# Optimization experiments

Measured on AMD Instinct MI355X. Metric: run time of the kernel, lower is better.

The kernel has to match this reference:

```python
import jax, jax.numpy as jnp
import numpy as np

N_NODES = 50000
N_EDGES = 500000
L_DIM = 128
MAX_ETYPES = 5
SELF_ETYPE = 4  # hardcoded in compute_edge_attention
K_FRAC = 0.5


def setup_inputs() -> dict:
    key = jax.random.key(0)
    ks = jax.random.split(key, 12)
    h = jax.random.normal(ks[0], (N_NODES, L_DIM), jnp.float32)
    src = jax.random.randint(ks[1], (N_EDGES,), 0, N_NODES)
    off = jax.random.randint(ks[2], (N_EDGES,), 1, N_NODES)
    dst = (src + off) % N_NODES  # guaranteed self-loop-free (remove_self_loop is a no-op)
    etype = jax.random.randint(ks[3], (N_EDGES,), 0, MAX_ETYPES)
    s = 0.05
    W_bases = jax.random.normal(ks[4], (2, 2 * L_DIM, L_DIM), jnp.float32) * s  # basis weights
    coeff = jax.random.normal(ks[5], (MAX_ETYPES, 2), jnp.float32)              # per-type basis coeffs
    Wq = jax.random.normal(ks[6], (L_DIM, L_DIM), jnp.float32) * s
    bq = jnp.zeros((L_DIM,), jnp.float32)
    Wk = jax.random.normal(ks[7], (L_DIM, L_DIM), jnp.float32) * s
    bk = jnp.zeros((L_DIM,), jnp.float32)
    Wv = jax.random.normal(ks[8], (1, L_DIM), jnp.float32) * s
    bv = jnp.zeros((1,), jnp.float32)
    return {"h": h, "src": src, "dst": dst, "etype": etype,
            "W_bases": W_bases, "coeff": coeff,
            "Wq": Wq, "bq": bq, "Wk": Wk, "bk": bk, "Wv": Wv, "bv": bv}


def typed_linear(x, et, W_bases, coeff):
    # basis-decomposed typed linear: W(t) = coeff[t,0]*W0 + coeff[t,1]*W1
    xW0 = x @ W_bases[0]
    xW1 = x @ W_bases[1]
    c = coeff[et]  # [E, 2]
    return c[:, 0:1] * xW0 + c[:, 1:2] * xW1


def reference(h, src, dst, etype, W_bases, coeff, Wq, bq, Wk, bk, Wv, bv):
    n, d = h.shape
    scale = jnp.sqrt(jnp.asarray(d, h.dtype))
    # self contribution: typed_linear([h, h], etype=4) -> w_v
    self_et = jnp.full((n,), SELF_ETYPE, dtype=jnp.int32)
    self_y = typed_linear(jnp.concatenate([h, h], axis=1), self_et, W_bases, coeff) @ Wv.T + bv  # [N,1]
    n_q = h @ Wq.T + bq  # [N, d]

    def direction(s_idx, d_idx):
        z2 = jnp.concatenate([h[s_idx], h[d_idx]], axis=1)          # [E, 2d]
        emb = typed_linear(z2, etype, W_bases, coeff)               # [E, d]
        n_k = emb @ Wk.T + bk                                       # [E, d]
        n_v = emb @ Wv.T + bv                                       # [E, 1]
        score = jnp.sum(n_k * n_q[d_idx], axis=-1, keepdims=True)   # [E, 1]
        score = jnp.exp(jnp.clip(score / scale, -10.0, 10.0))
        wV = jax.ops.segment_sum(score * n_v, d_idx, num_segments=n)  # [N,1]
        z = jax.ops.segment_sum(score, d_idx, num_segments=n)         # [N,1]
        return wV / (z + 1e-6)

    in_y = direction(src, dst)   # original graph, aggregate at dst
    out_y = direction(dst, src)  # reversed graph, aggregate at original src
    y = in_y + out_y + self_y    # [N,1] node attention

    # top-k pooling over a single graph (batch of 1): static keep size
    K = max(int(K_FRAC * n), 2)
    _, topk_idx = jax.lax.top_k(y[:, 0], K)
    sorted_node_ids = jnp.sort(topk_idx)          # original_node_ids of kept nodes
    perm = jnp.argsort(topk_idx)                  # == torch.sort(...).indices
    # NOTE: original code indexes node features with sort *positions* (0..K-1),
    # not node ids -- replicated faithfully.
    sel_y = y[perm]
    sel_h = h[perm]
    updated_h = sel_h * jax.nn.sigmoid(sel_y)     # dropout is identity at eval
    return updated_h, sorted_node_ids
```

## Files before the change

### kernel.cpp

```cpp
#include <hip/hip_runtime.h>
#include <hip/hip_bf16.h>
#include <math.h>

#define NN 50000
#define NE 500000
#define KSEL 25000

typedef unsigned int u32;
typedef unsigned long long u64;
typedef short bf16x8 __attribute__((ext_vector_type(8)));
typedef float f32x4 __attribute__((ext_vector_type(4)));

__device__ __forceinline__ unsigned short f2bf(float f) {
    u32 u = __float_as_uint(f);
    u32 r = (u + 0x7fffu + ((u >> 16) & 1u)) >> 16;
    return (unsigned short)r;
}
__device__ __forceinline__ float dpair(u32 a, u32 q) {
    float al = __uint_as_float(a << 16), ah = __uint_as_float(a & 0xffff0000u);
    float ql = __uint_as_float(q << 16), qh = __uint_as_float(q & 0xffff0000u);
    return al * ql + ah * qh;
}


__global__ __launch_bounds__(256) void k_cast(const float* __restrict__ h, unsigned short* __restrict__ hb) {
    int i = blockIdx.x * 256 + threadIdx.x;
    float4 v = *(const float4*)(h + (size_t)i * 4);
    ushort4 o;
    o.x = f2bf(v.x); o.y = f2bf(v.y); o.z = f2bf(v.z); o.w = f2bf(v.w);
    *(ushort4*)(hb + (size_t)i * 4) = o;
}

__global__ __launch_bounds__(128) void k_wqk(const float* __restrict__ Wq, const float* __restrict__ Wk,
                                             const float* __restrict__ bq,
                                             unsigned short* __restrict__ Gt, float* __restrict__ bqk) {
    int k = blockIdx.x;
    int m = threadIdx.x;
    float acc = 0.f;
    for (int c = 0; c < 128; ++c) acc += Wq[c * 128 + k] * Wk[c * 128 + m];
    Gt[(size_t)m * 128 + k] = f2bf(acc);
    if (k == 0) {
        float b = 0.f;
        for (int c = 0; c < 128; ++c) b += bq[c] * Wk[c * 128 + m];
        bqk[m] = b;
    }
}

__global__ void k_prep(const float* __restrict__ Wb, const float* __restrict__ Wq,
                       const float* __restrict__ bq, const float* __restrict__ bk,
                       const float* __restrict__ Wv,
                       unsigned short* __restrict__ Gt, float* __restrict__ wvecs) {
    int idx = blockIdx.x * blockDim.x + threadIdx.x;
    if (idx < 65536) {
        int p = idx >> 14, rem = idx & 16383;
        int c = rem >> 7, k = rem & 127;
        float v;
        if (p == 0)      v = Wb[k * 128 + c];
        else if (p == 1) v = Wb[32768 + k * 128 + c];
        else if (p == 2) v = Wb[16384 + k * 128 + c];
        else             v = Wb[49152 + k * 128 + c];
        Gt[(size_t)((p + 1) * 128 + c) * 128 + k] = f2bf(v);
    } else {
        int i = idx - 65536;
        if (i < 128)      { float s = 0; for (int m = 0; m < 128; ++m) s += Wb[i * 128 + m] * Wv[m]; wvecs[i] = s; }
        else if (i < 256) { int j = i - 128; float s = 0; for (int m = 0; m < 128; ++m) s += Wb[32768 + j * 128 + m] * Wv[m]; wvecs[i] = s; }
        else if (i < 384) { int j = i - 256; float s = 0; for (int m = 0; m < 128; ++m) s += Wb[(128 + j) * 128 + m] * Wv[m]; wvecs[i] = s; }
        else if (i < 512) { int j = i - 384; float s = 0; for (int m = 0; m < 128; ++m) s += Wb[32768 + (128 + j) * 128 + m] * Wv[m]; wvecs[i] = s; }
        else if (i < 640) { int j = i - 512; float s = 0; for (int c = 0; c < 128; ++c) s += bk[c] * Wq[c * 128 + j]; wvecs[i] = s; }
        else if (i == 640) { float s = 0; for (int c = 0; c < 128; ++c) s += bk[c] * bq[c]; wvecs[640] = s; }
    }
}

__global__ __launch_bounds__(256) void k_mfma(const unsigned short* __restrict__ hb,
                                              const unsigned short* __restrict__ Gt,
                                              const float* __restrict__ bqk,
                                              unsigned short* __restrict__ q2b,
                                              unsigned short* __restrict__ a01b,
                                              unsigned short* __restrict__ w0b,
                                              unsigned short* __restrict__ w1b) {
    int t = threadIdx.x;
    int w = t >> 6, l = t & 63;
    int lr = l & 15, lg = l >> 4;
    int mb = blockIdx.x * 128;
    int panel = blockIdx.y;
    int rowbase = mb + w * 32;

    bf16x8 afr[2][4];
#pragma unroll
    for (int rt = 0; rt < 2; ++rt)
#pragma unroll
        for (int kk = 0; kk < 4; ++kk) {
            int row = rowbase + rt * 16 + lr;
            if (row >= NN) row = NN - 1;
            afr[rt][kk] = *reinterpret_cast<const bf16x8*>(hb + (size_t)row * 128 + kk * 32 + lg * 8);
        }

    f32x4 acc[2][8];
#pragma unroll
    for (int rt = 0; rt < 2; ++rt)
#pragma unroll
        for (int ct = 0; ct < 8; ++ct) acc[rt][ct] = (f32x4){0.f, 0.f, 0.f, 0.f};

#pragma unroll
    for (int ct = 0; ct < 8; ++ct) {
#pragma unroll
        for (int kk = 0; kk < 4; ++kk) {
            int gcol = panel * 128 + ct * 16 + lr;
            bf16x8 bfr = *reinterpret_cast<const bf16x8*>(Gt + (size_t)gcol * 128 + kk * 32 + lg * 8);
            acc[0][ct] = __builtin_amdgcn_mfma_f32_16x16x32_bf16(afr[0][kk], bfr, acc[0][ct], 0, 0, 0);
            acc[1][ct] = __builtin_amdgcn_mfma_f32_16x16x32_bf16(afr[1][kk], bfr, acc[1][ct], 0, 0, 0);
        }
    }

#pragma unroll
    for (int rt = 0; rt < 2; ++rt)
#pragma unroll
        for (int ct = 0; ct < 8; ++ct)
#pragma unroll
            for (int r = 0; r < 4; ++r) {
                int row = rowbase + rt * 16 + lg * 4 + r;
                if (row >= NN) continue;
                int col = ct * 16 + lr;
                float v = acc[rt][ct][r];
                if (panel == 0) {
                    q2b[(size_t)row * 128 + col] = f2bf(v + bqk[col]);
                } else if (panel == 1) {
                    a01b[(size_t)row * 256 + col] = f2bf(v);
                } else if (panel == 2) {
                    a01b[(size_t)row * 256 + 128 + col] = f2bf(v);
                } else if (panel == 3) {
                    w0b[(size_t)row * 128 + col] = f2bf(v);
                } else {
                    w1b[(size_t)row * 128 + col] = f2bf(v);
                }
            }
}

__global__ __launch_bounds__(256) void k_tdot(const unsigned short* __restrict__ q2b,
                                              const unsigned short* __restrict__ w0b,
                                              const unsigned short* __restrict__ w1b,
                                              float* __restrict__ TT) {
    int n = blockIdx.x * 4 + (threadIdx.x >> 6);
    int lane = threadIdx.x & 63;
    u32 qw = ((const u32*)(q2b + (size_t)n * 128))[lane];
    u32 w0 = ((const u32*)(w0b + (size_t)n * 128))[lane];
    u32 w1 = ((const u32*)(w1b + (size_t)n * 128))[lane];
    float t0 = dpair(w0, qw);
    float t1 = dpair(w1, qw);
    for (int off = 32; off; off >>= 1) {
        t0 += __shfl_xor(t0, off);
        t1 += __shfl_xor(t1, off);
    }
    if (lane == 0) {
        TT[(size_t)n * 4 + 0] = t0;
        TT[(size_t)n * 4 + 1] = t1;
    }
}

__global__ void k_scal(const float* __restrict__ h, const float* __restrict__ wvecs,
                       const float* __restrict__ coeff, const float* __restrict__ bvp,
                       float* __restrict__ NS, float* __restrict__ TT, float* __restrict__ selfy) {
    int gid = blockIdx.x * blockDim.x + threadIdx.x;
    int wid = gid >> 6, lane = gid & 63;
    if (wid >= NN) return;
    const float* hrow = h + (size_t)wid * 128;
    float2 hv = *(const float2*)(hrow + lane * 2);
    float2 w0 = *(const float2*)(wvecs + 0 + lane * 2);
    float2 w1 = *(const float2*)(wvecs + 128 + lane * 2);
    float2 w2 = *(const float2*)(wvecs + 256 + lane * 2);
    float2 w3 = *(const float2*)(wvecs + 384 + lane * 2);
    float2 w4 = *(const float2*)(wvecs + 512 + lane * 2);
    float p0 = hv.x * w0.x + hv.y * w0.y;
    float p1 = hv.x * w1.x + hv.y * w1.y;
    float p2 = hv.x * w2.x + hv.y * w2.y;
    float p3 = hv.x * w3.x + hv.y * w3.y;
    float p4 = hv.x * w4.x + hv.y * w4.y;
    for (int off = 32; off; off >>= 1) {
        p0 += __shfl_xor(p0, off);
        p1 += __shfl_xor(p1, off);
        p2 += __shfl_xor(p2, off);
        p3 += __shfl_xor(p3, off);
        p4 += __shfl_xor(p4, off);
    }
    if (lane == 0) {
        float kn = p4 + wvecs[640];
        float c40 = coeff[8], c41 = coeff[9], bv = bvp[0];
        NS[(size_t)wid * 4 + 0] = p0;
        NS[(size_t)wid * 4 + 1] = p1;
        NS[(size_t)wid * 4 + 2] = p2;
        NS[(size_t)wid * 4 + 3] = p3;
        TT[(size_t)wid * 4 + 2] = kn;
        selfy[wid] = c40 * (p0 + p2) + c41 * (p1 + p3) + bv;
    }
}

__global__ __launch_bounds__(256) void k_edge(const unsigned short* __restrict__ a01b,
                                              const unsigned short* __restrict__ q2b,
                                              const int* __restrict__ src, const int* __restrict__ dst,
                                              const int* __restrict__ et,
                                              const float* __restrict__ NS, const float* __restrict__ TT,
                                              const float* __restrict__ coeff, const float* __restrict__ bvp,
                                              float* __restrict__ acc) {
    int tid = threadIdx.x;
    int e = blockIdx.x * 8 + (tid >> 5);
    int lane = tid & 63;
    int l5 = tid & 31;
    int g = l5 >> 3, sub = l5 & 7;
    int s = src[e], d = dst[e];
    int r1 = (g < 2) ? s : d;
    int r2 = (g < 2) ? d : s;
    const u32* ap = (const u32*)(a01b + (size_t)r1 * 256 + (g & 1) * 128) + sub * 8;
    const u32* qp = (const u32*)(q2b + (size_t)r2 * 128) + sub * 8;
    uint4 A0 = *(const uint4*)ap, A1 = *(const uint4*)(ap + 4);
    uint4 Q0 = *(const uint4*)qp, Q1 = *(const uint4*)(qp + 4);
    float p = dpair(A0.x, Q0.x) + dpair(A0.y, Q0.y) + dpair(A0.z, Q0.z) + dpair(A0.w, Q0.w) +
              dpair(A1.x, Q1.x) + dpair(A1.y, Q1.y) + dpair(A1.z, Q1.z) + dpair(A1.w, Q1.w);
    p += __shfl_xor(p, 4);
    p += __shfl_xor(p, 2);
    p += __shfl_xor(p, 1);
    float mate = __shfl(p, (lane + 8) & 63);
    if ((l5 & 15) == 0) {
        bool outdir = (l5 == 16);
        int agg = outdir ? s : d;
        int oth = outdir ? d : s;
        int ety = et[e];
        float c0 = coeff[ety * 2], c1 = coeff[ety * 2 + 1];
        float4 tt = *(const float4*)(TT + (size_t)agg * 4);
        float4 nsO = *(const float4*)(NS + (size_t)oth * 4);
        float4 nsA = *(const float4*)(NS + (size_t)agg * 4);
        float raw = c0 * (p + tt.x) + c1 * (mate + tt.y) + tt.z;
        float xc = fminf(fmaxf(raw * 0.08838834764831845f, -10.f), 10.f);
        float sc = expf(xc);
        float nv = c0 * (nsO.x + nsA.z) + c1 * (nsO.y + nsA.w) + bvp[0];
        float* wacc = acc + (size_t)(outdir ? 2 : 0) * NN;
        float* zacc = acc + (size_t)(outdir ? 3 : 1) * NN;
        atomicAdd(&wacc[agg], sc * nv);
        atomicAdd(&zacc[agg], sc);
    }
}


__global__ void k_y(const float* __restrict__ acc, const float* __restrict__ selfy,
                    float* __restrict__ y, u32* __restrict__ key, u32* __restrict__ hist) {
    int i = blockIdx.x * blockDim.x + threadIdx.x;
    if (i >= NN) return;
    float win = acc[i], zin = acc[NN + i], wout = acc[2 * NN + i], zout = acc[3 * NN + i];
    float v = win / (zin + 1e-6f) + wout / (zout + 1e-6f) + selfy[i];
    y[i] = v;
    u32 u = __float_as_uint(v);
    u32 m = (u32)((int)u >> 31) | 0x80000000u;
    u32 k = ~(u ^ m);
    key[i] = k;
    atomicAdd(&hist[k >> 16], 1u);
}

__global__ __launch_bounds__(1024) void k_scan(const u32* __restrict__ hist, u32* __restrict__ P) {
    __shared__ u32 wsum[16];
    __shared__ u32 woff[16];
    int t = threadIdx.x;
    int base = t * 64;
    u32 s = 0;
    for (int i = 0; i < 64; ++i) s += hist[base + i];
    u32 v = s;
    int lane = t & 63;
    for (int off = 1; off < 64; off <<= 1) {
        u32 n = __shfl_up(v, off);
        if (lane >= off) v += n;
    }
    int wid = t >> 6;
    if (lane == 63) wsum[wid] = v;
    __syncthreads();
    if (t == 0) {
        u32 r = 0;
        for (int w = 0; w < 16; ++w) { woff[w] = r; r += wsum[w]; }
    }
    __syncthreads();
    u32 excl = v - s + woff[wid];
    for (int i = 0; i < 64; ++i) { P[base + i] = excl; excl += hist[base + i]; }
    if (t == 1023) P[65536] = excl;
}

__global__ void k_scatter(const u32* __restrict__ key, const u32* __restrict__ P,
                          u32* __restrict__ cnt, u64* __restrict__ S) {
    int i = blockIdx.x * blockDim.x + threadIdx.x;
    if (i >= NN) return;
    u32 k = key[i];
    u32 b = k >> 16;
    u32 pos = P[b] + atomicAdd(&cnt[b], 1u);
    S[pos] = ((u64)k << 16) | (u32)i;
}

__global__ void k_rank(const u32* __restrict__ key, const u32* __restrict__ P,
                       const u64* __restrict__ S, u32* __restrict__ rnk) {
    int i = blockIdx.x * blockDim.x + threadIdx.x;
    if (i >= NN) return;
    u32 k = key[i];
    u32 b = k >> 16;
    u64 me = ((u64)k << 16) | (u32)i;
    u32 st = P[b], en = P[b + 1];
    u32 c = 0;
    for (u32 j = st; j < en; ++j) c += (S[j] < me) ? 1u : 0u;
    rnk[i] = st + c;
}

__global__ void k_bsum(const u32* __restrict__ rnk, u32* __restrict__ bs) {
    __shared__ u32 red[4];
    int i = blockIdx.x * 256 + threadIdx.x;
    u32 v = (i < NN && rnk[i] < KSEL) ? 1u : 0u;
    for (int off = 32; off; off >>= 1) v += __shfl_xor(v, off);
    int lane = threadIdx.x & 63, w = threadIdx.x >> 6;
    if (lane == 0) red[w] = v;
    __syncthreads();
    if (threadIdx.x == 0) bs[blockIdx.x] = red[0] + red[1] + red[2] + red[3];
}

__global__ void k_bscan(const u32* __restrict__ bs, u32* __restrict__ bo, int nb) {
    if (threadIdx.x == 0) {
        u32 r = 0;
        for (int i = 0; i < nb; ++i) { bo[i] = r; r += bs[i]; }
    }
}

__global__ void k_select(const u32* __restrict__ rnk, const u32* __restrict__ bo,
                         u32* __restrict__ selj, float* __restrict__ out_ids) {
    __shared__ u32 woff[4];
    int t = threadIdx.x;
    int i = blockIdx.x * 256 + t;
    u32 f = (i < NN && rnk[i] < KSEL) ? 1u : 0u;
    u32 v = f;
    int lane = t & 63;
    for (int off = 1; off < 64; off <<= 1) {
        u32 n = __shfl_up(v, off);
        if (lane >= off) v += n;
    }
    int w = t >> 6;
    if (lane == 63) woff[w] = v;
    __syncthreads();
    if (t == 0) {
        u32 r = 0;
        for (int k = 0; k < 4; ++k) { u32 x = woff[k]; woff[k] = r; r += x; }
    }
    __syncthreads();
    if (f) {
        u32 r = bo[blockIdx.x] + woff[w] + (v - f);
        selj[r] = rnk[i];
        out_ids[r] = (float)i;
    }
}

__global__ void k_rows(const u32* __restrict__ selj, const float* __restrict__ h,
                       const float* __restrict__ y, float* __restrict__ out) {
    int row = blockIdx.x * 2 + (threadIdx.x >> 7);
    int c = threadIdx.x & 127;
    if (row >= KSEL) return;
    u32 j = selj[row];
    float yv = y[j];
    float sig = 1.f / (1.f + expf(-yv));
    float v = h[(size_t)j * 128 + c] * sig;
    out[(size_t)row * 128 + c] = v;
}


extern "C" void kernel_launch(void* const* d_in, const int* in_sizes, int n_in,
                              void* d_out, int out_size, void* d_ws, size_t ws_size,
                              hipStream_t stream) {
    const float* h    = (const float*)d_in[0];
    const int* src    = (const int*)d_in[1];
    const int* dstp   = (const int*)d_in[2];
    const int* etype  = (const int*)d_in[3];
    const float* Wb   = (const float*)d_in[4];
    const float* coeff = (const float*)d_in[5];
    const float* Wq   = (const float*)d_in[6];
    const float* bq   = (const float*)d_in[7];
    const float* Wk   = (const float*)d_in[8];
    const float* bk   = (const float*)d_in[9];
    const float* Wv   = (const float*)d_in[10];
    const float* bv   = (const float*)d_in[11];

    char* ws = (char*)d_ws;
    size_t off = 0;
    auto alloc = [&](size_t bytes) -> void* {
        void* p = ws + off;
        off = (off + bytes + 255) & ~(size_t)255;
        return p;
    };
    unsigned short* hb   = (unsigned short*)alloc((size_t)NN * 128 * 2);
    unsigned short* Gt   = (unsigned short*)alloc((size_t)640 * 128 * 2);
    unsigned short* q2b  = (unsigned short*)alloc((size_t)NN * 128 * 2);
    unsigned short* a01b = (unsigned short*)alloc((size_t)NN * 256 * 2);
    unsigned short* w0b  = (unsigned short*)alloc((size_t)NN * 128 * 2);
    unsigned short* w1b  = (unsigned short*)alloc((size_t)NN * 128 * 2);
    float* bqk   = (float*)alloc(128 * 4);
    float* wvecs = (float*)alloc(644 * 4);
    float* NS    = (float*)alloc((size_t)NN * 4 * 4);
    float* TT    = (float*)alloc((size_t)NN * 4 * 4);
    float* selfy = (float*)alloc((size_t)NN * 4);
    float* y     = (float*)alloc((size_t)NN * 4);
    u32* key     = (u32*)alloc((size_t)NN * 4);
    u64* S       = (u64*)alloc((size_t)NN * 8);
    u32* rnk     = (u32*)alloc((size_t)NN * 4);
    u32* selj    = (u32*)alloc((size_t)KSEL * 4);
    u32* bs      = (u32*)alloc(256 * 4);
    u32* bo      = (u32*)alloc(256 * 4);
    u32* P       = (u32*)alloc(65537 * 4);
    size_t zstart = off;
    float* acc = (float*)alloc((size_t)NN * 4 * 4);
    u32* hist  = (u32*)alloc(65536 * 4);
    u32* cnt   = (u32*)alloc(65536 * 4);
    size_t zend = off;
    (void)ws_size; (void)n_in; (void)in_sizes; (void)out_size;

    hipMemsetAsync(ws + zstart, 0, zend - zstart, stream);

    k_cast<<<(NN * 128 / 4 + 255) / 256, 256, 0, stream>>>(h, hb);
    k_wqk<<<128, 128, 0, stream>>>(Wq, Wk, bq, Gt, bqk);
    k_prep<<<(65536 + 641 + 255) / 256, 256, 0, stream>>>(Wb, Wq, bq, bk, Wv, Gt, wvecs);
    k_mfma<<<dim3((NN + 127) / 128, 5), 256, 0, stream>>>(hb, Gt, bqk, q2b, a01b, w0b, w1b);
    k_tdot<<<(NN + 3) / 4, 256, 0, stream>>>(q2b, w0b, w1b, TT);
    k_scal<<<(NN * 64 + 255) / 256, 256, 0, stream>>>(h, wvecs, coeff, bv, NS, TT, selfy);
    k_edge<<<NE / 8, 256, 0, stream>>>(a01b, q2b, src, dstp, etype, NS, TT, coeff, bv, acc);
    int nb = (NN + 255) / 256;
    k_y<<<nb, 256, 0, stream>>>(acc, selfy, y, key, hist);
    k_scan<<<1, 1024, 0, stream>>>(hist, P);
    k_scatter<<<nb, 256, 0, stream>>>(key, P, cnt, S);
    k_rank<<<nb, 256, 0, stream>>>(key, P, S, rnk);
    k_bsum<<<nb, 256, 0, stream>>>(rnk, bs);
    k_bscan<<<1, 64, 0, stream>>>(bs, bo, nb);
    float* out = (float*)d_out;
    k_select<<<nb, 256, 0, stream>>>(rnk, bo, selj, out + (size_t)KSEL * 128);
    k_rows<<<(KSEL + 1) / 2, 256, 0, stream>>>(selj, h, y, out);
}
```

Baseline: 429.1 us.

## Bucket edges by destination block and pack edge fields for locality

Adds a counting-sort pass (histogram, scan, scatter) that groups edges into 128-node destination buckets. It packs src, dst and etype into one 64-bit word per edge, which k_edge now reads instead of three separate arrays. The aim is better cache locality for the dst-side gathers and the per-node atomic accumulations. The cost is three extra launches and heavily contended atomics on only 391 bucket counters. Separately, k_scan now caches its histogram slice in registers with vector loads, and k_bscan becomes a parallel wave scan instead of a single-thread loop.

```diff
diff --git a/kernel.cpp b/kernel.cpp
--- a/kernel.cpp
+++ b/kernel.cpp
@@ -5,6 +5,7 @@
 #define NN 50000
 #define NE 500000
 #define KSEL 25000
+#define NB_E 391
 
 typedef unsigned int u32;
 typedef unsigned long long u64;
@@ -194,10 +195,42 @@
     }
 }
 
+
+__global__ void k_ehist(const int* __restrict__ dst, u32* __restrict__ ecnt) {
+    int e = blockIdx.x * 256 + threadIdx.x;
+    if (e < NE) atomicAdd(&ecnt[((u32)dst[e]) >> 7], 1u);
+}
+
+__global__ __launch_bounds__(512) void k_escan(const u32* __restrict__ ecnt, u32* __restrict__ eoff) {
+    __shared__ u32 ws[8];
+    int t = threadIdx.x;
+    u32 x = (t < NB_E) ? ecnt[t] : 0;
+    u32 v = x;
+    int lane = t & 63;
+    for (int o = 1; o < 64; o <<= 1) { u32 n = __shfl_up(v, o); if (lane >= o) v += n; }
+    int w = t >> 6;
+    if (lane == 63) ws[w] = v;
+    __syncthreads();
+    if (t == 0) { u32 r = 0; for (int i = 0; i < 8; ++i) { u32 q = ws[i]; ws[i] = r; r += q; } }
+    __syncthreads();
+    v += ws[w];
+    if (t <= NB_E) eoff[t] = v - x;
+}
+
+__global__ void k_escat(const int* __restrict__ src, const int* __restrict__ dst,
+                        const int* __restrict__ et, const u32* __restrict__ eoff,
+                        u32* __restrict__ ecnt2, u64* __restrict__ EP) {
+    int e = blockIdx.x * 256 + threadIdx.x;
+    if (e >= NE) return;
+    u32 d = (u32)dst[e];
+    u32 b = d >> 7;
+    u32 pos = eoff[b] + atomicAdd(&ecnt2[b], 1u);
+    EP[pos] = (u64)(u32)src[e] | ((u64)d << 16) | ((u64)(u32)et[e] << 32);
+}
+
 __global__ __launch_bounds__(256) void k_edge(const unsigned short* __restrict__ a01b,
                                               const unsigned short* __restrict__ q2b,
-                                              const int* __restrict__ src, const int* __restrict__ dst,
-                                              const int* __restrict__ et,
+                                              const u64* __restrict__ EP,
                                               const float* __restrict__ NS, const float* __restrict__ TT,
                                               const float* __restrict__ coeff, const float* __restrict__ bvp,
                                               float* __restrict__ acc) {
@@ -206,7 +239,10 @@
     int lane = tid & 63;
     int l5 = tid & 31;
     int g = l5 >> 3, sub = l5 & 7;
-    int s = src[e], d = dst[e];
+    u64 wrd = EP[e];
+    int s = (int)(wrd & 0xFFFF);
+    int d = (int)((wrd >> 16) & 0xFFFF);
+    int ety = (int)((wrd >> 32) & 0x7);
     int r1 = (g < 2) ? s : d;
     int r2 = (g < 2) ? d : s;
     const u32* ap = (const u32*)(a01b + (size_t)r1 * 256 + (g & 1) * 128) + sub * 8;
@@ -223,7 +259,6 @@
         bool outdir = (l5 == 16);
         int agg = outdir ? s : d;
         int oth = outdir ? d : s;
-        int ety = et[e];
         float c0 = coeff[ety * 2], c1 = coeff[ety * 2 + 1];
         float4 tt = *(const float4*)(TT + (size_t)agg * 4);
         float4 nsO = *(const float4*)(NS + (size_t)oth * 4);
@@ -259,8 +294,12 @@
     __shared__ u32 woff[16];
     int t = threadIdx.x;
     int base = t * 64;
+    u32 hv[64];
+#pragma unroll
+    for (int i = 0; i < 16; ++i) *(uint4*)&hv[i * 4] = ((const uint4*)(hist + base))[i];
     u32 s = 0;
-    for (int i = 0; i < 64; ++i) s += hist[base + i];
+#pragma unroll
+    for (int i = 0; i < 64; ++i) s += hv[i];
     u32 v = s;
     int lane = t & 63;
     for (int off = 1; off < 64; off <<= 1) {
@@ -276,7 +315,8 @@
     }
     __syncthreads();
     u32 excl = v - s + woff[wid];
-    for (int i = 0; i < 64; ++i) { P[base + i] = excl; excl += hist[base + i]; }
+#pragma unroll
+    for (int i = 0; i < 64; ++i) { P[base + i] = excl; excl += hv[i]; }
     if (t == 1023) P[65536] = excl;
 }
 
@@ -314,11 +354,19 @@
     if (threadIdx.x == 0) bs[blockIdx.x] = red[0] + red[1] + red[2] + red[3];
 }
 
-__global__ void k_bscan(const u32* __restrict__ bs, u32* __restrict__ bo, int nb) {
-    if (threadIdx.x == 0) {
-        u32 r = 0;
-        for (int i = 0; i < nb; ++i) { bo[i] = r; r += bs[i]; }
-    }
+__global__ __launch_bounds__(256) void k_bscan(const u32* __restrict__ bs, u32* __restrict__ bo, int nb) {
+    __shared__ u32 ws[4];
+    int t = threadIdx.x;
+    u32 x = (t < nb) ? bs[t] : 0;
+    u32 v = x;
+    int lane = t & 63;
+    for (int o = 1; o < 64; o <<= 1) { u32 n = __shfl_up(v, o); if (lane >= o) v += n; }
+    int w = t >> 6;
+    if (lane == 63) ws[w] = v;
+    __syncthreads();
+    if (t == 0) { u32 r = 0; for (int i = 0; i < 4; ++i) { u32 q = ws[i]; ws[i] = r; r += q; } }
+    __syncthreads();
+    if (t < nb) bo[t] = v + ws[w] - x;
 }
 
 __global__ void k_select(const u32* __restrict__ rnk, const u32* __restrict__ bo,
@@ -390,6 +438,8 @@
     unsigned short* a01b = (unsigned short*)alloc((size_t)NN * 256 * 2);
     unsigned short* w0b  = (unsigned short*)alloc((size_t)NN * 128 * 2);
     unsigned short* w1b  = (unsigned short*)alloc((size_t)NN * 128 * 2);
+    u64* EP      = (u64*)alloc((size_t)NE * 8);
+    u32* eoff    = (u32*)alloc((NB_E + 1) * 4);
     float* bqk   = (float*)alloc(128 * 4);
     float* wvecs = (float*)alloc(644 * 4);
     float* NS    = (float*)alloc((size_t)NN * 4 * 4);
@@ -407,6 +457,8 @@
     float* acc = (float*)alloc((size_t)NN * 4 * 4);
     u32* hist  = (u32*)alloc(65536 * 4);
     u32* cnt   = (u32*)alloc(65536 * 4);
+    u32* ecnt  = (u32*)alloc((NB_E + 1) * 4);
+    u32* ecnt2 = (u32*)alloc((NB_E + 1) * 4);
     size_t zend = off;
     (void)ws_size; (void)n_in; (void)in_sizes; (void)out_size;
 
@@ -415,17 +467,20 @@
     k_cast<<<(NN * 128 / 4 + 255) / 256, 256, 0, stream>>>(h, hb);
     k_wqk<<<128, 128, 0, stream>>>(Wq, Wk, bq, Gt, bqk);
     k_prep<<<(65536 + 641 + 255) / 256, 256, 0, stream>>>(Wb, Wq, bq, bk, Wv, Gt, wvecs);
+    k_ehist<<<(NE + 255) / 256, 256, 0, stream>>>(dstp, ecnt);
+    k_escan<<<1, 512, 0, stream>>>(ecnt, eoff);
+    k_escat<<<(NE + 255) / 256, 256, 0, stream>>>(src, dstp, etype, eoff, ecnt2, EP);
     k_mfma<<<dim3((NN + 127) / 128, 5), 256, 0, stream>>>(hb, Gt, bqk, q2b, a01b, w0b, w1b);
     k_tdot<<<(NN + 3) / 4, 256, 0, stream>>>(q2b, w0b, w1b, TT);
     k_scal<<<(NN * 64 + 255) / 256, 256, 0, stream>>>(h, wvecs, coeff, bv, NS, TT, selfy);
-    k_edge<<<NE / 8, 256, 0, stream>>>(a01b, q2b, src, dstp, etype, NS, TT, coeff, bv, acc);
+    k_edge<<<NE / 8, 256, 0, stream>>>(a01b, q2b, EP, NS, TT, coeff, bv, acc);
     int nb = (NN + 255) / 256;
     k_y<<<nb, 256, 0, stream>>>(acc, selfy, y, key, hist);
     k_scan<<<1, 1024, 0, stream>>>(hist, P);
     k_scatter<<<nb, 256, 0, stream>>>(key, P, cnt, S);
     k_rank<<<nb, 256, 0, stream>>>(key, P, S, rnk);
     k_bsum<<<nb, 256, 0, stream>>>(rnk, bs);
-    k_bscan<<<1, 64, 0, stream>>>(bs, bo, nb);
+    k_bscan<<<1, 256, 0, stream>>>(bs, bo, nb);
     float* out = (float*)d_out;
     k_select<<<nb, 256, 0, stream>>>(rnk, bo, selj, out + (size_t)KSEL * 128);
     k_rows<<<(KSEL + 1) / 2, 256, 0, stream>>>(selj, h, y, out);
```

After: 791.2 us. 1.84x slower.

## Fuse node-side GEMM, bf16 cast, scalar projections and T-dots into one kernel

Applied to the files above, without the earlier changes.

Merges the cast, five-panel MFMA GEMM, per-node dot products (k_tdot) and scalar projections (k_scal) into a single k_node kernel. It reads fp32 h directly, keeps the q2k tile in registers, and computes the w0/w1 dot products in-register, so the w0b/w1b intermediates are never written. The three weight-prep kernels become one, rank and block-sum are fused, and the block offset scan moves into k_select, removing several launches. The cost is higher register pressure and longer per-block serial work in k_node, since each block now computes all five panels.

```diff
diff --git a/kernel.cpp b/kernel.cpp
--- a/kernel.cpp
+++ b/kernel.cpp
@@ -21,38 +21,27 @@
     float ql = __uint_as_float(q << 16), qh = __uint_as_float(q & 0xffff0000u);
     return al * ql + ah * qh;
 }
-
-
-__global__ __launch_bounds__(256) void k_cast(const float* __restrict__ h, unsigned short* __restrict__ hb) {
-    int i = blockIdx.x * 256 + threadIdx.x;
-    float4 v = *(const float4*)(h + (size_t)i * 4);
-    ushort4 o;
-    o.x = f2bf(v.x); o.y = f2bf(v.y); o.z = f2bf(v.z); o.w = f2bf(v.w);
-    *(ushort4*)(hb + (size_t)i * 4) = o;
-}
-
-__global__ __launch_bounds__(128) void k_wqk(const float* __restrict__ Wq, const float* __restrict__ Wk,
-                                             const float* __restrict__ bq,
-                                             unsigned short* __restrict__ Gt, float* __restrict__ bqk) {
-    int k = blockIdx.x;
-    int m = threadIdx.x;
-    float acc = 0.f;
-    for (int c = 0; c < 128; ++c) acc += Wq[c * 128 + k] * Wk[c * 128 + m];
-    Gt[(size_t)m * 128 + k] = f2bf(acc);
-    if (k == 0) {
-        float b = 0.f;
-        for (int c = 0; c < 128; ++c) b += bq[c] * Wk[c * 128 + m];
-        bqk[m] = b;
-    }
-}
-
-__global__ void k_prep(const float* __restrict__ Wb, const float* __restrict__ Wq,
-                       const float* __restrict__ bq, const float* __restrict__ bk,
-                       const float* __restrict__ Wv,
-                       unsigned short* __restrict__ Gt, float* __restrict__ wvecs) {
+__device__ __forceinline__ bf16x8 pack8(float4 a, float4 b) {
+    bf16x8 r;
+    r[0] = (short)f2bf(a.x); r[1] = (short)f2bf(a.y); r[2] = (short)f2bf(a.z); r[3] = (short)f2bf(a.w);
+    r[4] = (short)f2bf(b.x); r[5] = (short)f2bf(b.y); r[6] = (short)f2bf(b.z); r[7] = (short)f2bf(b.w);
+    return r;
+}
+
+__global__ void k_prep2(const float* __restrict__ Wq, const float* __restrict__ Wk,
+                        const float* __restrict__ bq, const float* __restrict__ bk,
+                        const float* __restrict__ Wv, const float* __restrict__ Wb,
+                        unsigned short* __restrict__ Gt, float* __restrict__ bqk,
+                        float* __restrict__ wvecs) {
     int idx = blockIdx.x * blockDim.x + threadIdx.x;
-    if (idx < 65536) {
-        int p = idx >> 14, rem = idx & 16383;
+    if (idx < 16384) {
+        int k = idx >> 7, m = idx & 127;
+        float acc = 0.f;
+        for (int c = 0; c < 128; ++c) acc += Wq[c * 128 + k] * Wk[c * 128 + m];
+        Gt[(size_t)m * 128 + k] = f2bf(acc);
+    } else if (idx < 16384 + 65536) {
+        int i = idx - 16384;
+        int p = i >> 14, rem = i & 16383;
         int c = rem >> 7, k = rem & 127;
         float v;
         if (p == 0)      v = Wb[k * 128 + c];
@@ -61,136 +50,178 @@
         else             v = Wb[49152 + k * 128 + c];
         Gt[(size_t)((p + 1) * 128 + c) * 128 + k] = f2bf(v);
     } else {
-        int i = idx - 65536;
-        if (i < 128)      { float s = 0; for (int m = 0; m < 128; ++m) s += Wb[i * 128 + m] * Wv[m]; wvecs[i] = s; }
-        else if (i < 256) { int j = i - 128; float s = 0; for (int m = 0; m < 128; ++m) s += Wb[32768 + j * 128 + m] * Wv[m]; wvecs[i] = s; }
-        else if (i < 384) { int j = i - 256; float s = 0; for (int m = 0; m < 128; ++m) s += Wb[(128 + j) * 128 + m] * Wv[m]; wvecs[i] = s; }
-        else if (i < 512) { int j = i - 384; float s = 0; for (int m = 0; m < 128; ++m) s += Wb[32768 + (128 + j) * 128 + m] * Wv[m]; wvecs[i] = s; }
-        else if (i < 640) { int j = i - 512; float s = 0; for (int c = 0; c < 128; ++c) s += bk[c] * Wq[c * 128 + j]; wvecs[i] = s; }
-        else if (i == 640) { float s = 0; for (int c = 0; c < 128; ++c) s += bk[c] * bq[c]; wvecs[640] = s; }
-    }
-}
-
-__global__ __launch_bounds__(256) void k_mfma(const unsigned short* __restrict__ hb,
+        int i = idx - 16384 - 65536;
+        if (i < 128) { float b = 0; for (int c = 0; c < 128; ++c) b += bq[c] * Wk[c * 128 + i]; bqk[i] = b; }
+        else {
+            int j = i - 128;
+            if (j < 128)      { float s = 0; for (int m = 0; m < 128; ++m) s += Wb[j * 128 + m] * Wv[m]; wvecs[j] = s; }
+            else if (j < 256) { int q = j - 128; float s = 0; for (int m = 0; m < 128; ++m) s += Wb[32768 + q * 128 + m] * Wv[m]; wvecs[j] = s; }
+            else if (j < 384) { int q = j - 256; float s = 0; for (int m = 0; m < 128; ++m) s += Wb[(128 + q) * 128 + m] * Wv[m]; wvecs[j] = s; }
+            else if (j < 512) { int q = j - 384; float s = 0; for (int m = 0; m < 128; ++m) s += Wb[32768 + (128 + q) * 128 + m] * Wv[m]; wvecs[j] = s; }
+            else if (j < 640) { int q = j - 512; float s = 0; for (int c = 0; c < 128; ++c) s += bk[c] * Wq[c * 128 + q]; wvecs[j] = s; }
+            else if (j == 640) { float s = 0; for (int c = 0; c < 128; ++c) s += bk[c] * bq[c]; wvecs[640] = s; }
+        }
+    }
+}
+
+__global__ __launch_bounds__(256) void k_node(const float* __restrict__ h,
                                               const unsigned short* __restrict__ Gt,
                                               const float* __restrict__ bqk,
+                                              const float* __restrict__ wvecs,
+                                              const float* __restrict__ coeff,
+                                              const float* __restrict__ bvp,
                                               unsigned short* __restrict__ q2b,
                                               unsigned short* __restrict__ a01b,
-                                              unsigned short* __restrict__ w0b,
-                                              unsigned short* __restrict__ w1b) {
+                                              float* __restrict__ NS, float* __restrict__ TT,
+                                              float* __restrict__ selfy) {
     int t = threadIdx.x;
     int w = t >> 6, l = t & 63;
     int lr = l & 15, lg = l >> 4;
-    int mb = blockIdx.x * 128;
-    int panel = blockIdx.y;
-    int rowbase = mb + w * 32;
+    int rowbase = blockIdx.x * 128 + w * 32;
 
     bf16x8 afr[2][4];
+    float ns[2][5];
 #pragma unroll
     for (int rt = 0; rt < 2; ++rt)
 #pragma unroll
-        for (int kk = 0; kk < 4; ++kk) {
+        for (int c = 0; c < 5; ++c) ns[rt][c] = 0.f;
+
+#pragma unroll
+    for (int kk = 0; kk < 4; ++kk) {
+        float4 wvA[5], wvB[5];
+#pragma unroll
+        for (int c = 0; c < 5; ++c) {
+            const float* wv = wvecs + c * 128 + kk * 32 + lg * 8;
+            wvA[c] = *(const float4*)wv;
+            wvB[c] = *(const float4*)(wv + 4);
+        }
+#pragma unroll
+        for (int rt = 0; rt < 2; ++rt) {
             int row = rowbase + rt * 16 + lr;
             if (row >= NN) row = NN - 1;
-            afr[rt][kk] = *reinterpret_cast<const bf16x8*>(hb + (size_t)row * 128 + kk * 32 + lg * 8);
-        }
+            const float* hp = h + (size_t)row * 128 + kk * 32 + lg * 8;
+            float4 a = *(const float4*)hp;
+            float4 b = *(const float4*)(hp + 4);
+#pragma unroll
+            for (int c = 0; c < 5; ++c) {
+                ns[rt][c] += a.x * wvA[c].x + a.y * wvA[c].y + a.z * wvA[c].z + a.w * wvA[c].w +
+                             b.x * wvB[c].x + b.y * wvB[c].y + b.z * wvB[c].z + b.w * wvB[c].w;
+            }
+            afr[rt][kk] = pack8(a, b);
+        }
+    }
+#pragma unroll
+    for (int rt = 0; rt < 2; ++rt)
+#pragma unroll
+        for (int c = 0; c < 5; ++c) {
+            ns[rt][c] += __shfl_xor(ns[rt][c], 16);
+            ns[rt][c] += __shfl_xor(ns[rt][c], 32);
+        }
+    if (lg == 0) {
+        float c40 = coeff[8], c41 = coeff[9], bv = bvp[0], bkbq = wvecs[640];
+#pragma unroll
+        for (int rt = 0; rt < 2; ++rt) {
+            int row = rowbase + rt * 16 + lr;
+            if (row < NN) {
+                NS[(size_t)row * 4 + 0] = ns[rt][0];
+                NS[(size_t)row * 4 + 1] = ns[rt][1];
+                NS[(size_t)row * 4 + 2] = ns[rt][2];
+                NS[(size_t)row * 4 + 3] = ns[rt][3];
+                TT[(size_t)row * 4 + 2] = ns[rt][4] + bkbq;
+                selfy[row] = c40 * (ns[rt][0] + ns[rt][2]) + c41 * (ns[rt][1] + ns[rt][3]) + bv;
+            }
+        }
+    }
 
     f32x4 acc[2][8];
-#pragma unroll
-    for (int rt = 0; rt < 2; ++rt)
-#pragma unroll
-        for (int ct = 0; ct < 8; ++ct) acc[rt][ct] = (f32x4){0.f, 0.f, 0.f, 0.f};
+    f32x4 q2k[2][8];
 
 #pragma unroll
     for (int ct = 0; ct < 8; ++ct) {
+        acc[0][ct] = (f32x4){0.f, 0.f, 0.f, 0.f};
+        acc[1][ct] = (f32x4){0.f, 0.f, 0.f, 0.f};
 #pragma unroll
         for (int kk = 0; kk < 4; ++kk) {
-            int gcol = panel * 128 + ct * 16 + lr;
-            bf16x8 bfr = *reinterpret_cast<const bf16x8*>(Gt + (size_t)gcol * 128 + kk * 32 + lg * 8);
+            bf16x8 bfr = *reinterpret_cast<const bf16x8*>(Gt + (size_t)(ct * 16 + lr) * 128 + kk * 32 + lg * 8);
             acc[0][ct] = __builtin_amdgcn_mfma_f32_16x16x32_bf16(afr[0][kk], bfr, acc[0][ct], 0, 0, 0);
             acc[1][ct] = __builtin_amdgcn_mfma_f32_16x16x32_bf16(afr[1][kk], bfr, acc[1][ct], 0, 0, 0);
         }
     }
-
 #pragma unroll
     for (int rt = 0; rt < 2; ++rt)
 #pragma unroll
-        for (int ct = 0; ct < 8; ++ct)
+        for (int ct = 0; ct < 8; ++ct) {
+            float bb = bqk[ct * 16 + lr];
 #pragma unroll
             for (int r = 0; r < 4; ++r) {
                 int row = rowbase + rt * 16 + lg * 4 + r;
-                if (row >= NN) continue;
-                int col = ct * 16 + lr;
-                float v = acc[rt][ct][r];
-                if (panel == 0) {
-                    q2b[(size_t)row * 128 + col] = f2bf(v + bqk[col]);
-                } else if (panel == 1) {
-                    a01b[(size_t)row * 256 + col] = f2bf(v);
-                } else if (panel == 2) {
-                    a01b[(size_t)row * 256 + 128 + col] = f2bf(v);
-                } else if (panel == 3) {
-                    w0b[(size_t)row * 128 + col] = f2bf(v);
-                } else {
-                    w1b[(size_t)row * 128 + col] = f2bf(v);
+                float v = acc[rt][ct][r] + bb;
+                q2k[rt][ct][r] = v;
+                if (row < NN) q2b[(size_t)row * 128 + ct * 16 + lr] = f2bf(v);
+            }
+        }
+
+#pragma unroll
+    for (int pn = 1; pn <= 2; ++pn) {
+#pragma unroll
+        for (int ct = 0; ct < 8; ++ct) {
+            acc[0][ct] = (f32x4){0.f, 0.f, 0.f, 0.f};
+            acc[1][ct] = (f32x4){0.f, 0.f, 0.f, 0.f};
+#pragma unroll
+            for (int kk = 0; kk < 4; ++kk) {
+                bf16x8 bfr = *reinterpret_cast<const bf16x8*>(Gt + (size_t)(pn * 128 + ct * 16 + lr) * 128 + kk * 32 + lg * 8);
+                acc[0][ct] = __builtin_amdgcn_mfma_f32_16x16x32_bf16(afr[0][kk], bfr, acc[0][ct], 0, 0, 0);
+                acc[1][ct] = __builtin_amdgcn_mfma_f32_16x16x32_bf16(afr[1][kk], bfr, acc[1][ct], 0, 0, 0);
+            }
+        }
+        int cbase = (pn == 1) ? 0 : 128;
+#pragma unroll
+        for (int rt = 0; rt < 2; ++rt)
+#pragma unroll
+            for (int ct = 0; ct < 8; ++ct)
+#pragma unroll
+                for (int r = 0; r < 4; ++r) {
+                    int row = rowbase + rt * 16 + lg * 4 + r;
+                    if (row < NN) a01b[(size_t)row * 256 + cbase + ct * 16 + lr] = f2bf(acc[rt][ct][r]);
                 }
-            }
-}
-
-__global__ __launch_bounds__(256) void k_tdot(const unsigned short* __restrict__ q2b,
-                                              const unsigned short* __restrict__ w0b,
-                                              const unsigned short* __restrict__ w1b,
-                                              float* __restrict__ TT) {
-    int n = blockIdx.x * 4 + (threadIdx.x >> 6);
-    int lane = threadIdx.x & 63;
-    u32 qw = ((const u32*)(q2b + (size_t)n * 128))[lane];
-    u32 w0 = ((const u32*)(w0b + (size_t)n * 128))[lane];
-    u32 w1 = ((const u32*)(w1b + (size_t)n * 128))[lane];
-    float t0 = dpair(w0, qw);
-    float t1 = dpair(w1, qw);
-    for (int off = 32; off; off >>= 1) {
-        t0 += __shfl_xor(t0, off);
-        t1 += __shfl_xor(t1, off);
-    }
-    if (lane == 0) {
-        TT[(size_t)n * 4 + 0] = t0;
-        TT[(size_t)n * 4 + 1] = t1;
-    }
-}
-
-__global__ void k_scal(const float* __restrict__ h, const float* __restrict__ wvecs,
-                       const float* __restrict__ coeff, const float* __restrict__ bvp,
-                       float* __restrict__ NS, float* __restrict__ TT, float* __restrict__ selfy) {
-    int gid = blockIdx.x * blockDim.x + threadIdx.x;
-    int wid = gid >> 6, lane = gid & 63;
-    if (wid >= NN) return;
-    const float* hrow = h + (size_t)wid * 128;
-    float2 hv = *(const float2*)(hrow + lane * 2);
-    float2 w0 = *(const float2*)(wvecs + 0 + lane * 2);
-    float2 w1 = *(const float2*)(wvecs + 128 + lane * 2);
-    float2 w2 = *(const float2*)(wvecs + 256 + lane * 2);
-    float2 w3 = *(const float2*)(wvecs + 384 + lane * 2);
-    float2 w4 = *(const float2*)(wvecs + 512 + lane * 2);
-    float p0 = hv.x * w0.x + hv.y * w0.y;
-    float p1 = hv.x * w1.x + hv.y * w1.y;
-    float p2 = hv.x * w2.x + hv.y * w2.y;
-    float p3 = hv.x * w3.x + hv.y * w3.y;
-    float p4 = hv.x * w4.x + hv.y * w4.y;
-    for (int off = 32; off; off >>= 1) {
-        p0 += __shfl_xor(p0, off);
-        p1 += __shfl_xor(p1, off);
-        p2 += __shfl_xor(p2, off);
-        p3 += __shfl_xor(p3, off);
-        p4 += __shfl_xor(p4, off);
-    }
-    if (lane == 0) {
-        float kn = p4 + wvecs[640];
-        float c40 = coeff[8], c41 = coeff[9], bv = bvp[0];
-        NS[(size_t)wid * 4 + 0] = p0;
-        NS[(size_t)wid * 4 + 1] = p1;
-        NS[(size_t)wid * 4 + 2] = p2;
-        NS[(size_t)wid * 4 + 3] = p3;
-        TT[(size_t)wid * 4 + 2] = kn;
-        selfy[wid] = c40 * (p0 + p2) + c41 * (p1 + p3) + bv;
+    }
+
+#pragma unroll
+    for (int pn = 3; pn <= 4; ++pn) {
+#pragma unroll
+        for (int ct = 0; ct < 8; ++ct) {
+            acc[0][ct] = (f32x4){0.f, 0.f, 0.f, 0.f};
+            acc[1][ct] = (f32x4){0.f, 0.f, 0.f, 0.f};
+#pragma unroll
+            for (int kk = 0; kk < 4; ++kk) {
+                bf16x8 bfr = *reinterpret_cast<const bf16x8*>(Gt + (size_t)(pn * 128 + ct * 16 + lr) * 128 + kk * 32 + lg * 8);
+                acc[0][ct] = __builtin_amdgcn_mfma_f32_16x16x32_bf16(afr[0][kk], bfr, acc[0][ct], 0, 0, 0);
+                acc[1][ct] = __builtin_amdgcn_mfma_f32_16x16x32_bf16(afr[1][kk], bfr, acc[1][ct], 0, 0, 0);
+            }
+        }
+        float tp[2][4];
+#pragma unroll
+        for (int rt = 0; rt < 2; ++rt)
+#pragma unroll
+            for (int r = 0; r < 4; ++r) {
+                float s = 0.f;
+#pragma unroll
+                for (int ct = 0; ct < 8; ++ct) s += q2k[rt][ct][r] * acc[rt][ct][r];
+                s += __shfl_xor(s, 1);
+                s += __shfl_xor(s, 2);
+                s += __shfl_xor(s, 4);
+                s += __shfl_xor(s, 8);
+                tp[rt][r] = s;
+            }
+        if (lr == 0) {
+#pragma unroll
+            for (int rt = 0; rt < 2; ++rt)
+#pragma unroll
+                for (int r = 0; r < 4; ++r) {
+                    int row = rowbase + rt * 16 + lg * 4 + r;
+                    if (row < NN) TT[(size_t)row * 4 + (pn - 3)] = tp[rt][r];
+                }
+        }
     }
 }
 
@@ -259,8 +290,12 @@
     __shared__ u32 woff[16];
     int t = threadIdx.x;
     int base = t * 64;
+    u32 hv[64];
+#pragma unroll
+    for (int i = 0; i < 16; ++i) *(uint4*)&hv[i * 4] = ((const uint4*)(hist + base))[i];
     u32 s = 0;
-    for (int i = 0; i < 64; ++i) s += hist[base + i];
+#pragma unroll
+    for (int i = 0; i < 64; ++i) s += hv[i];
     u32 v = s;
     int lane = t & 63;
     for (int off = 1; off < 64; off <<= 1) {
@@ -276,7 +311,8 @@
     }
     __syncthreads();
     u32 excl = v - s + woff[wid];
-    for (int i = 0; i < 64; ++i) { P[base + i] = excl; excl += hist[base + i]; }
+#pragma unroll
+    for (int i = 0; i < 64; ++i) { P[base + i] = excl; excl += hv[i]; }
     if (t == 1023) P[65536] = excl;
 }
 
@@ -291,58 +327,55 @@
 }
 
 __global__ void k_rank(const u32* __restrict__ key, const u32* __restrict__ P,
-                       const u64* __restrict__ S, u32* __restrict__ rnk) {
-    int i = blockIdx.x * blockDim.x + threadIdx.x;
-    if (i >= NN) return;
-    u32 k = key[i];
-    u32 b = k >> 16;
-    u64 me = ((u64)k << 16) | (u32)i;
-    u32 st = P[b], en = P[b + 1];
-    u32 c = 0;
-    for (u32 j = st; j < en; ++j) c += (S[j] < me) ? 1u : 0u;
-    rnk[i] = st + c;
-}
-
-__global__ void k_bsum(const u32* __restrict__ rnk, u32* __restrict__ bs) {
+                       const u64* __restrict__ S, u32* __restrict__ rnk, u32* __restrict__ bs) {
     __shared__ u32 red[4];
     int i = blockIdx.x * 256 + threadIdx.x;
-    u32 v = (i < NN && rnk[i] < KSEL) ? 1u : 0u;
-    for (int off = 32; off; off >>= 1) v += __shfl_xor(v, off);
+    u32 f = 0;
+    if (i < NN) {
+        u32 k = key[i];
+        u32 b = k >> 16;
+        u64 me = ((u64)k << 16) | (u32)i;
+        u32 st = P[b], en = P[b + 1];
+        u32 c = 0;
+        for (u32 j = st; j < en; ++j) c += (S[j] < me) ? 1u : 0u;
+        u32 r = st + c;
+        rnk[i] = r;
+        f = (r < KSEL) ? 1u : 0u;
+    }
+    for (int off = 32; off; off >>= 1) f += __shfl_xor(f, off);
     int lane = threadIdx.x & 63, w = threadIdx.x >> 6;
-    if (lane == 0) red[w] = v;
+    if (lane == 0) red[w] = f;
     __syncthreads();
     if (threadIdx.x == 0) bs[blockIdx.x] = red[0] + red[1] + red[2] + red[3];
 }
 
-__global__ void k_bscan(const u32* __restrict__ bs, u32* __restrict__ bo, int nb) {
-    if (threadIdx.x == 0) {
-        u32 r = 0;
-        for (int i = 0; i < nb; ++i) { bo[i] = r; r += bs[i]; }
-    }
-}
-
-__global__ void k_select(const u32* __restrict__ rnk, const u32* __restrict__ bo,
-                         u32* __restrict__ selj, float* __restrict__ out_ids) {
-    __shared__ u32 woff[4];
+__global__ __launch_bounds__(256) void k_select(const u32* __restrict__ rnk, const u32* __restrict__ bs,
+                                                u32* __restrict__ selj, float* __restrict__ out_ids, int nb) {
+    __shared__ u32 sc[256];
+    __shared__ u32 aux[4];
+    __shared__ u32 aux2[4];
     int t = threadIdx.x;
+    int lane = t & 63, w = t >> 6;
+    u32 x = (t < nb) ? bs[t] : 0;
+    u32 v = x;
+    for (int o = 1; o < 64; o <<= 1) { u32 n = __shfl_up(v, o); if (lane >= o) v += n; }
+    if (lane == 63) aux[w] = v;
+    __syncthreads();
+    if (t == 0) { u32 r = 0; for (int k = 0; k < 4; ++k) { u32 q = aux[k]; aux[k] = r; r += q; } }
+    __syncthreads();
+    sc[t] = v + aux[w] - x;
+    __syncthreads();
+    u32 base = sc[blockIdx.x];
     int i = blockIdx.x * 256 + t;
     u32 f = (i < NN && rnk[i] < KSEL) ? 1u : 0u;
-    u32 v = f;
-    int lane = t & 63;
-    for (int off = 1; off < 64; off <<= 1) {
-        u32 n = __shfl_up(v, off);
-        if (lane >= off) v += n;
-    }
-    int w = t >> 6;
-    if (lane == 63) woff[w] = v;
-    __syncthreads();
-    if (t == 0) {
-        u32 r = 0;
-        for (int k = 0; k < 4; ++k) { u32 x = woff[k]; woff[k] = r; r += x; }
-    }
+    u32 vv = f;
+    for (int o = 1; o < 64; o <<= 1) { u32 n = __shfl_up(vv, o); if (lane >= o) vv += n; }
+    if (lane == 63) aux2[w] = vv;
+    __syncthreads();
+    if (t == 0) { u32 r = 0; for (int k = 0; k < 4; ++k) { u32 q = aux2[k]; aux2[k] = r; r += q; } }
     __syncthreads();
     if (f) {
-        u32 r = bo[blockIdx.x] + woff[w] + (v - f);
+        u32 r = base + aux2[w] + (vv - f);
         selj[r] = rnk[i];
         out_ids[r] = (float)i;
     }
@@ -384,12 +417,9 @@
         off = (off + bytes + 255) & ~(size_t)255;
         return p;
     };
-    unsigned short* hb   = (unsigned short*)alloc((size_t)NN * 128 * 2);
     unsigned short* Gt   = (unsigned short*)alloc((size_t)640 * 128 * 2);
     unsigned short* q2b  = (unsigned short*)alloc((size_t)NN * 128 * 2);
     unsigned short* a01b = (unsigned short*)alloc((size_t)NN * 256 * 2);
-    unsigned short* w0b  = (unsigned short*)alloc((size_t)NN * 128 * 2);
-    unsigned short* w1b  = (unsigned short*)alloc((size_t)NN * 128 * 2);
     float* bqk   = (float*)alloc(128 * 4);
     float* wvecs = (float*)alloc(644 * 4);
     float* NS    = (float*)alloc((size_t)NN * 4 * 4);
@@ -401,7 +431,6 @@
     u32* rnk     = (u32*)alloc((size_t)NN * 4);
     u32* selj    = (u32*)alloc((size_t)KSEL * 4);
     u32* bs      = (u32*)alloc(256 * 4);
-    u32* bo      = (u32*)alloc(256 * 4);
     u32* P       = (u32*)alloc(65537 * 4);
     size_t zstart = off;
     float* acc = (float*)alloc((size_t)NN * 4 * 4);
@@ -412,21 +441,15 @@
 
     hipMemsetAsync(ws + zstart, 0, zend - zstart, stream);
 
-    k_cast<<<(NN * 128 / 4 + 255) / 256, 256, 0, stream>>>(h, hb);
-    k_wqk<<<128, 128, 0, stream>>>(Wq, Wk, bq, Gt, bqk);
-    k_prep<<<(65536 + 641 + 255) / 256, 256, 0, stream>>>(Wb, Wq, bq, bk, Wv, Gt, wvecs);
-    k_mfma<<<dim3((NN + 127) / 128, 5), 256, 0, stream>>>(hb, Gt, bqk, q2b, a01b, w0b, w1b);
-    k_tdot<<<(NN + 3) / 4, 256, 0, stream>>>(q2b, w0b, w1b, TT);
-    k_scal<<<(NN * 64 + 255) / 256, 256, 0, stream>>>(h, wvecs, coeff, bv, NS, TT, selfy);
+    k_prep2<<<(16384 + 65536 + 769 + 255) / 256, 256, 0, stream>>>(Wq, Wk, bq, bk, Wv, Wb, Gt, bqk, wvecs);
+    k_node<<<(NN + 127) / 128, 256, 0, stream>>>(h, Gt, bqk, wvecs, coeff, bv, q2b, a01b, NS, TT, selfy);
     k_edge<<<NE / 8, 256, 0, stream>>>(a01b, q2b, src, dstp, etype, NS, TT, coeff, bv, acc);
     int nb = (NN + 255) / 256;
     k_y<<<nb, 256, 0, stream>>>(acc, selfy, y, key, hist);
     k_scan<<<1, 1024, 0, stream>>>(hist, P);
     k_scatter<<<nb, 256, 0, stream>>>(key, P, cnt, S);
-    k_rank<<<nb, 256, 0, stream>>>(key, P, S, rnk);
-    k_bsum<<<nb, 256, 0, stream>>>(rnk, bs);
-    k_bscan<<<1, 64, 0, stream>>>(bs, bo, nb);
+    k_rank<<<nb, 256, 0, stream>>>(key, P, S, rnk, bs);
     float* out = (float*)d_out;
-    k_select<<<nb, 256, 0, stream>>>(rnk, bo, selj, out + (size_t)KSEL * 128);
+    k_select<<<nb, 256, 0, stream>>>(rnk, bs, selj, out + (size_t)KSEL * 128, nb);
     k_rows<<<(KSEL + 1) / 2, 256, 0, stream>>>(selj, h, y, out);
 }
```

New measurement: 395.9 us. 1.08x faster.
